# Performance work log

Measured on AMD Instinct MI355X. Metric: run time of the kernel, lower is better.

Reference implementation:

```python
import jax, jax.numpy as jnp
import numpy as np


def _im2col(x, hf, wf, pad, dilation):
    """Dilated im2col, stride 1, CS231n layout.

    x: (N, C, H, W) -> cols: (C, hf*wf, H*W*N) where the last axis is ordered
    (h, w, n), i.e. index = (h*W + w)*N + n, matching the torch im2col_indices
    helper used by Infuse.
    """
    n, c, h, w = x.shape
    xp = jnp.pad(x, ((0, 0), (0, 0), (pad, pad), (pad, pad)))
    # fixed small loop over the hf*wf window offsets (25 for ksize=5)
    patches = jnp.stack(
        [xp[:, :, i * dilation:i * dilation + h, j * dilation:j * dilation + w]
         for i in range(hf) for j in range(wf)], axis=2)  # (N, C, K2, H, W)
    return patches.transpose(1, 2, 3, 4, 0).reshape(c, hf * wf, h * w * n)


def setup_inputs() -> dict:
    key = jax.random.key(0)
    k1, k2, k3 = jax.random.split(key, 3)
    N, D, H, W, K = 2, 64, 128, 128, 5
    V = jax.random.normal(k1, (N, D, H, W), dtype=jnp.float32)
    boundary = jax.random.uniform(k2, (N, 1, H, W), dtype=jnp.float32)
    dist_to_center = jax.random.uniform(k3, (K * K,), dtype=jnp.float32)
    return {"V": V, "boundary": boundary, "ksize": 5, "dilation": 3,
            "dist_to_center": dist_to_center}


def reference(V, boundary, ksize, dilation, dist_to_center):
    n, d, h, w = V.shape
    pad = (ksize // 2) * dilation
    k2 = ksize * ksize

    # im2col_boundary: gather dilated boundary patches and weight each window
    # offset by its distance to the window center (clipped to a valid boundary
    # probability in [0, 1]).
    bcols = _im2col(boundary, ksize, ksize, pad, dilation)[0]  # (K2, H*W*N)
    boundary_max = jnp.clip(bcols * dist_to_center[:, None], 0.0, 1.0)

    # boundary-proximity attention over the local window
    boundary_sim = 1.0 - boundary_max + 1e-5                   # (K2, H*W*N)
    att = boundary_sim / jnp.sum(boundary_sim, axis=0, keepdims=True)
    # zero-out (scale down) attention at pixels that are themselves boundary
    att = att * (1.0 - boundary).transpose(1, 2, 3, 0).reshape(-1)[None, :]

    # gather feature patches and reduce over the window
    vcols = _im2col(V, ksize, ksize, pad, dilation)            # (D, K2, H*W*N)
    out = (vcols * att[None]).sum(axis=1)                      # (D, H*W*N)
    return out.reshape(d, h, w, n).transpose(3, 0, 1, 2)       # (N, D, H, W)
```

## Files before the change

### kernel.cpp

```cpp
#include <hip/hip_runtime.h>

constexpr int N = 2, D = 64, H = 128, W = 128;
constexpr int K = 5, K2 = 25, DIL = 3, PAD = 6;
constexpr int DCHUNK = 16;
constexpr int HW = H * W;
constexpr int VBYTES = N * D * H * W * 4;
constexpr int SK2 = 36;
constexpr int WATT = 26 * SK2;

typedef float float4v __attribute__((ext_vector_type(4)));
typedef float float2v __attribute__((ext_vector_type(2)));

__device__ __forceinline__ void pk_fma(float2v& d, float2v s0, float2v s1) {
    asm("v_pk_fma_f32 %0, %1, %2, %0" : "+v"(d) : "v"(s0), "v"(s1));
}

__global__ __launch_bounds__(256, 4)
void infuse_kernel(const float* __restrict__ V,
                   const float* __restrict__ boundary,
                   const float* __restrict__ dist,
                   float* __restrict__ out) {
    int obid = blockIdx.x;
    int bid  = (obid & 7) * 128 + (obid >> 3);
    int dblk = bid & 3;
    int h    = (bid >> 2) & (H - 1);
    int n    = bid >> 9;

    __shared__ float s_att[4 * WATT];

    int tid  = threadIdx.x;
    int wv   = tid >> 6;
    int lane = tid & 63;
    float* watt = &s_att[wv * WATT];

    int g   = lane & 3;
    int c   = lane >> 2;
    int d   = dblk * DCHUNK + c;
    int px0 = 32 * wv + 8 * g;

    int cb   = (n * D + d) * (H * W * 4);
    int colb = px0 * 4 - 32;
    const char* Vb = (const char*)V;

    float4v pre[2][6];
#pragma unroll
    for (int i = 0; i < 2; ++i) {
        int r  = h + i * DIL - PAD;
        int rb = cb + r * (W * 4) + colb;
#pragma unroll
        for (int e = 0; e < 6; ++e) {
            int o = rb + 16 * e;
            o = min(max(o, 0), VBYTES - 16);
            pre[i][e] = *(const float4v*)(Vb + o);
        }
    }
    __builtin_amdgcn_sched_barrier(0);

    {
        int pxl  = lane & 31;
        int wpx  = 32 * wv + pxl;
        int half = lane >> 5;
        const float* bp = boundary + n * HW;
        float bc = bp[h * W + wpx];

        float bvr[13];
        bool  ok[13];
#pragma unroll
        for (int kk = 0; kk < 13; ++kk) {
            const int iA = kk / 5,        jA = kk % 5;
            const int iB = (kk + 13) / 5, jB = (kk + 13) % 5;
            int idel = half ? (iB * DIL - PAD) : (iA * DIL - PAD);
            int jdel = half ? (jB * DIL - PAD) : (jA * DIL - PAD);
            int bh = h + idel;
            int bw = wpx + jdel;
            bool inb = (bh >= 0) & (bh < H) & (bw >= 0) & (bw < W);
            if (kk == 12) inb = inb & (half == 0);
            ok[kk] = inb;
            int off = bh * W + bw;
            off = min(max(off, 0), HW - 1);
            bvr[kk] = bp[off];
        }
        float sv[13];
        float partial = 0.f;
#pragma unroll
        for (int kk = 0; kk < 13; ++kk) {
            float dA = dist[kk];
            float dB = (kk < 12) ? dist[kk + 13] : 0.f;
            float dk = half ? dB : dA;
            float bv = ok[kk] ? bvr[kk] : 0.f;
            float bm = fminf(fmaxf(bv * dk, 0.f), 1.f);
            float s  = 1.f - bm + 1e-5f;
            partial += (kk == 12) ? (half ? 0.f : s) : s;
            sv[kk] = s;
        }
        float other = __shfl_xor(partial, 32);
        float total = partial + other;
        float scale = (1.f - bc) / total;
        float* sb = watt + half * 13 * SK2 + pxl;
#pragma unroll
        for (int kk = 0; kk < 13; ++kk)
            sb[kk * SK2] = ok[kk] ? sv[kk] * scale : 0.f;
    }
    asm volatile("s_waitcnt lgkmcnt(0)" ::: "memory");
    __builtin_amdgcn_sched_barrier(0);

    float2v acc2[4] = {{0,0},{0,0},{0,0},{0,0}};
    const float* ar = watt + 8 * g;

#pragma unroll
    for (int i = 0; i < K; ++i) {
        float4v v[6];
        if (i < 2) {
#pragma unroll
            for (int e = 0; e < 6; ++e) v[e] = pre[i][e];
        } else {
            int r  = h + i * DIL - PAD;
            int rb = cb + r * (W * 4) + colb;
#pragma unroll
            for (int e = 0; e < 6; ++e) {
                int o = rb + 16 * e;
                o = min(max(o, 0), VBYTES - 16);
                v[e] = *(const float4v*)(Vb + o);
            }
        }
#pragma unroll
        for (int j = 0; j < K; ++j) {
            const float* ap = ar + (i * K + j) * SK2;
            float4v aLo = *(const float4v*)ap;
            float4v aHi = *(const float4v*)(ap + 4);
            if ((j & 1) == 0) {
#pragma unroll
                for (int pp = 0; pp < 4; ++pp) {
                    const int idx = 2 * pp + 3 * j + 2;
                    float2v s0 = {v[idx >> 2][idx & 3],
                                  v[(idx + 1) >> 2][(idx + 1) & 3]};
                    float2v a2 = (pp < 2) ? float2v{aLo[2*pp], aLo[2*pp+1]}
                                          : float2v{aHi[2*pp-4], aHi[2*pp-3]};
                    pk_fma(acc2[pp], s0, a2);
                }
            } else {
#pragma unroll
                for (int px = 0; px < 8; ++px) {
                    const int idx = px + 3 * j + 2;
                    float a = (px < 4) ? aLo[px & 3] : aHi[px & 3];
                    acc2[px >> 1][px & 1] =
                        fmaf(v[idx >> 2][idx & 3], a, acc2[px >> 1][px & 1]);
                }
            }
        }
    }

    float4v o0 = {acc2[0][0], acc2[0][1], acc2[1][0], acc2[1][1]};
    float4v o1 = {acc2[2][0], acc2[2][1], acc2[3][0], acc2[3][1]};

    size_t ob = ((size_t)(n * D + d) * H + h) * W + px0;
    *(float4v*)(out + ob)     = o0;
    *(float4v*)(out + ob + 4) = o1;
}

extern "C" void kernel_launch(void* const* d_in, const int* in_sizes, int n_in,
                              void* d_out, int out_size, void* d_ws, size_t ws_size,
                              hipStream_t stream) {
    const float* V        = (const float*)d_in[0];
    const float* boundary = (const float*)d_in[1];
    const float* dist     = (const float*)d_in[4];
    float* out = (float*)d_out;

    int grid = N * H * (D / DCHUNK);
    infuse_kernel<<<grid, 256, 0, stream>>>(V, boundary, dist, out);
}
```

Measured before the change: 12.38 us.

## Raise occupancy, drop V prefetch, defer attention normalization to output

```diff
diff --git a/kernel.cpp b/kernel.cpp
--- a/kernel.cpp
+++ b/kernel.cpp
@@ -15,7 +15,7 @@
     asm("v_pk_fma_f32 %0, %1, %2, %0" : "+v"(d) : "v"(s0), "v"(s1));
 }
 
-__global__ __launch_bounds__(256, 4)
+__global__ __launch_bounds__(256, 8)
 void infuse_kernel(const float* __restrict__ V,
                    const float* __restrict__ boundary,
                    const float* __restrict__ dist,
@@ -42,26 +42,11 @@
     int colb = px0 * 4 - 32;
     const char* Vb = (const char*)V;
 
-    float4v pre[2][6];
-#pragma unroll
-    for (int i = 0; i < 2; ++i) {
-        int r  = h + i * DIL - PAD;
-        int rb = cb + r * (W * 4) + colb;
-#pragma unroll
-        for (int e = 0; e < 6; ++e) {
-            int o = rb + 16 * e;
-            o = min(max(o, 0), VBYTES - 16);
-            pre[i][e] = *(const float4v*)(Vb + o);
-        }
-    }
-    __builtin_amdgcn_sched_barrier(0);
-
     {
         int pxl  = lane & 31;
         int wpx  = 32 * wv + pxl;
         int half = lane >> 5;
         const float* bp = boundary + n * HW;
-        float bc = bp[h * W + wpx];
 
         float bvr[13];
         bool  ok[13];
@@ -80,8 +65,8 @@
             off = min(max(off, 0), HW - 1);
             bvr[kk] = bp[off];
         }
-        float sv[13];
         float partial = 0.f;
+        float* sb = watt + half * 13 * SK2 + pxl;
 #pragma unroll
         for (int kk = 0; kk < 13; ++kk) {
             float dA = dist[kk];
@@ -91,15 +76,10 @@
             float bm = fminf(fmaxf(bv * dk, 0.f), 1.f);
             float s  = 1.f - bm + 1e-5f;
             partial += (kk == 12) ? (half ? 0.f : s) : s;
-            sv[kk] = s;
+            sb[kk * SK2] = ok[kk] ? s : 0.f;
         }
-        float other = __shfl_xor(partial, 32);
-        float total = partial + other;
-        float scale = (1.f - bc) / total;
-        float* sb = watt + half * 13 * SK2 + pxl;
-#pragma unroll
-        for (int kk = 0; kk < 13; ++kk)
-            sb[kk * SK2] = ok[kk] ? sv[kk] * scale : 0.f;
+        float total = partial + __shfl_xor(partial, 32);
+        if (!half) watt[25 * SK2 + pxl] = (1.f - bvr[12]) / total;
     }
     asm volatile("s_waitcnt lgkmcnt(0)" ::: "memory");
     __builtin_amdgcn_sched_barrier(0);
@@ -110,18 +90,13 @@
 #pragma unroll
     for (int i = 0; i < K; ++i) {
         float4v v[6];
-        if (i < 2) {
+        int r  = h + i * DIL - PAD;
+        int rb = cb + r * (W * 4) + colb;
 #pragma unroll
-            for (int e = 0; e < 6; ++e) v[e] = pre[i][e];
-        } else {
-            int r  = h + i * DIL - PAD;
-            int rb = cb + r * (W * 4) + colb;
-#pragma unroll
-            for (int e = 0; e < 6; ++e) {
-                int o = rb + 16 * e;
-                o = min(max(o, 0), VBYTES - 16);
-                v[e] = *(const float4v*)(Vb + o);
-            }
+        for (int e = 0; e < 6; ++e) {
+            int o = rb + 16 * e;
+            o = min(max(o, 0), VBYTES - 16);
+            v[e] = *(const float4v*)(Vb + o);
         }
 #pragma unroll
         for (int j = 0; j < K; ++j) {
@@ -150,8 +125,13 @@
         }
     }
 
-    float4v o0 = {acc2[0][0], acc2[0][1], acc2[1][0], acc2[1][1]};
-    float4v o1 = {acc2[2][0], acc2[2][1], acc2[3][0], acc2[3][1]};
+    const float* sp = watt + 25 * SK2 + 8 * g;
+    float4v scLo = *(const float4v*)sp;
+    float4v scHi = *(const float4v*)(sp + 4);
+    float4v o0 = {acc2[0][0] * scLo[0], acc2[0][1] * scLo[1],
+                  acc2[1][0] * scLo[2], acc2[1][1] * scLo[3]};
+    float4v o1 = {acc2[2][0] * scHi[0], acc2[2][1] * scHi[1],
+                  acc2[3][0] * scHi[2], acc2[3][1] * scHi[3]};
 
     size_t ob = ((size_t)(n * D + d) * H + h) * W + px0;
     *(float4v*)(out + ob)     = o0;
```

New measurement: 12.88 us. +4.0%, slower.
